# Kernel optimization log

Measured on AMD Instinct MI355X. Metric: run time of the kernel, lower is better.

The kernel has to match this reference:

```python
import jax, jax.numpy as jnp
import numpy as np

B, H, S, D = 4, 16, 2048, 64

def setup_inputs() -> dict:
    key = jax.random.key(0)
    kq, kk, kv = jax.random.split(key, 3)
    q = jax.random.normal(kq, (B, H, S, D), dtype=jnp.float32)
    k = jax.random.normal(kk, (B, H, S, D), dtype=jnp.float32)
    v = jax.random.normal(kv, (B, H, S, D), dtype=jnp.float32)
    return {"q": q, "k": k, "v": v}

def reference(q, k, v):
    # Faithful port of TransformerBlock.scaled_dot_product_attention
    # (is_causal=True, mha_dropout=0.0 / eval mode).
    head_dim = q.shape[-1]
    scale = jnp.asarray(head_dim, q.dtype) ** -0.5
    q_len, k_len = q.shape[-2], k.shape[-2]
    # causal additive bias: 0 on/below diagonal, -inf above
    causal = jnp.tril(jnp.ones((q_len, k_len), dtype=bool))
    attn_bias = jnp.where(causal, jnp.asarray(0.0, q.dtype), jnp.asarray(-jnp.inf, q.dtype))
    # [b,h,s,d] x [b,h,t,d] -> [b,h,s,t]
    attn_weights = jnp.einsum('bhsd,bhtd->bhst', q * scale, k) + attn_bias
    attn = jax.nn.softmax(attn_weights, axis=-1)
    out = jnp.einsum('bhst,bhtd->bhsd', attn, v)
    return out
```

## Files before the change

kernel.cpp:

```cpp
#include <hip/hip_runtime.h>
#include <math.h>


#define S_LEN 2048
#define D_DIM 64
#define TK 64
#define LSTR 72
#define MNEG -30000.0f

typedef __attribute__((ext_vector_type(8))) short bf16x8;
typedef __attribute__((ext_vector_type(4))) float f32x4;

static __device__ __forceinline__ float fast_exp2(float x) {
#if __has_builtin(__builtin_amdgcn_exp2f)
    return __builtin_amdgcn_exp2f(x);
#else
    float r;
    asm volatile("v_exp_f32 %0, %1\n\ts_nop 1" : "=v"(r) : "v"(x));
    return r;
#endif
}

static __device__ __forceinline__ unsigned int pack_bf16(float a, float b) {
    union { float f; unsigned int u; } ca, cb;
    ca.f = a; cb.f = b;
    unsigned int ua = ca.u + 0x8000u;
    unsigned int ub = cb.u + 0x8000u;
    return (ua >> 16) | (ub & 0xFFFF0000u);
}

__global__ __launch_bounds__(256, 4)
void fa_fwd(const float* __restrict__ qg,
            const float* __restrict__ kg,
            const float* __restrict__ vg,
            float* __restrict__ og)
{
    const int head = blockIdx.x;
    const int pr   = blockIdx.y;
    const int tid  = threadIdx.x;
    const int wave = tid >> 6;
    const int lane = tid & 63;
    const int m16  = lane & 15;
    const int quad = lane >> 4;

    __shared__ unsigned short Kl[TK][LSTR];
    __shared__ unsigned short Vt[D_DIM][LSTR];
    __shared__ unsigned short Pl[4][16][LSTR];

    const size_t hoff = (size_t)head * S_LEN * D_DIM;
    const float* kh = kg + hoff;
    const float* vh = vg + hoff;

    const int ksr = tid >> 2;
    const int ksc = (tid & 3) << 4;
    const int va  = lane >> 3;
    const int vb  = lane & 7;
    const int vrr = wave * 16 + 2 * vb;
    const int vcc = 8 * va;
    const float LOG2E = 1.4426950408889634f;

    for (int pass = 0; pass < 2; ++pass) {
        const int q0 = ((pass == 0) ? pr : (31 - pr)) * TK;

        bf16x8 qf[2];
        {
            const float* qp = qg + hoff + (size_t)(q0 + wave * 16 + m16) * D_DIM + quad * 8;
            #pragma unroll
            for (int c = 0; c < 2; ++c) {
                float4 a = reinterpret_cast<const float4*>(qp + c * 32)[0];
                float4 b = reinterpret_cast<const float4*>(qp + c * 32)[1];
                unsigned int u0 = pack_bf16(a.x * 0.125f, a.y * 0.125f);
                unsigned int u1 = pack_bf16(a.z * 0.125f, a.w * 0.125f);
                unsigned int u2 = pack_bf16(b.x * 0.125f, b.y * 0.125f);
                unsigned int u3 = pack_bf16(b.z * 0.125f, b.w * 0.125f);
                qf[c][0] = (short)(u0 & 0xFFFF); qf[c][1] = (short)(u0 >> 16);
                qf[c][2] = (short)(u1 & 0xFFFF); qf[c][3] = (short)(u1 >> 16);
                qf[c][4] = (short)(u2 & 0xFFFF); qf[c][5] = (short)(u2 >> 16);
                qf[c][6] = (short)(u3 & 0xFFFF); qf[c][7] = (short)(u3 >> 16);
            }
        }

        float m_i = MNEG, l_i = 0.f;
        f32x4 oacc[4];
        #pragma unroll
        for (int nc = 0; nc < 4; ++nc) oacc[nc] = (f32x4){0.f, 0.f, 0.f, 0.f};

        float4 kA, kB, kC, kD, vA, vB, vC, vD;
        {
            const float* kp = kh + (size_t)ksr * D_DIM + ksc;
            kA = reinterpret_cast<const float4*>(kp)[0];
            kB = reinterpret_cast<const float4*>(kp)[1];
            kC = reinterpret_cast<const float4*>(kp)[2];
            kD = reinterpret_cast<const float4*>(kp)[3];
            const float* vp = vh + (size_t)vrr * D_DIM + vcc;
            vA = reinterpret_cast<const float4*>(vp)[0];
            vB = reinterpret_cast<const float4*>(vp)[1];
            vC = reinterpret_cast<const float4*>(vp + D_DIM)[0];
            vD = reinterpret_cast<const float4*>(vp + D_DIM)[1];
        }

        for (int j0 = 0; j0 <= q0; j0 += TK) {
            __syncthreads();
            {
                uint4 w0, w1;
                w0.x = pack_bf16(kA.x, kA.y); w0.y = pack_bf16(kA.z, kA.w);
                w0.z = pack_bf16(kB.x, kB.y); w0.w = pack_bf16(kB.z, kB.w);
                w1.x = pack_bf16(kC.x, kC.y); w1.y = pack_bf16(kC.z, kC.w);
                w1.z = pack_bf16(kD.x, kD.y); w1.w = pack_bf16(kD.z, kD.w);
                *reinterpret_cast<uint4*>(&Kl[ksr][ksc])     = w0;
                *reinterpret_cast<uint4*>(&Kl[ksr][ksc + 8]) = w1;

                float r0[8] = {vA.x, vA.y, vA.z, vA.w, vB.x, vB.y, vB.z, vB.w};
                float r1[8] = {vC.x, vC.y, vC.z, vC.w, vD.x, vD.y, vD.z, vD.w};
                #pragma unroll
                for (int jj = 0; jj < 8; ++jj) {
                    int j = (jj + va) & 7;
                    *reinterpret_cast<unsigned int*>(&Vt[vcc + j][vrr]) = pack_bf16(r0[j], r1[j]);
                }
            }
            __syncthreads();

            if (j0 + TK <= q0) {
                const float* kp = kh + (size_t)(j0 + TK + ksr) * D_DIM + ksc;
                kA = reinterpret_cast<const float4*>(kp)[0];
                kB = reinterpret_cast<const float4*>(kp)[1];
                kC = reinterpret_cast<const float4*>(kp)[2];
                kD = reinterpret_cast<const float4*>(kp)[3];
                const float* vp = vh + (size_t)(j0 + TK + vrr) * D_DIM + vcc;
                vA = reinterpret_cast<const float4*>(vp)[0];
                vB = reinterpret_cast<const float4*>(vp)[1];
                vC = reinterpret_cast<const float4*>(vp + D_DIM)[0];
                vD = reinterpret_cast<const float4*>(vp + D_DIM)[1];
            }

            float sv[4][4];
            #pragma unroll
            for (int nt = 0; nt < 4; ++nt) {
                f32x4 acc = (f32x4){0.f, 0.f, 0.f, 0.f};
                bf16x8 kf0 = *reinterpret_cast<const bf16x8*>(&Kl[nt * 16 + m16][quad * 8]);
                bf16x8 kf1 = *reinterpret_cast<const bf16x8*>(&Kl[nt * 16 + m16][32 + quad * 8]);
                acc = __builtin_amdgcn_mfma_f32_16x16x32_bf16(kf0, qf[0], acc, 0, 0, 0);
                acc = __builtin_amdgcn_mfma_f32_16x16x32_bf16(kf1, qf[1], acc, 0, 0, 0);
                #pragma unroll
                for (int r = 0; r < 4; ++r) sv[nt][r] = acc[r];
            }

            if (j0 == q0) {
                #pragma unroll
                for (int nt = 0; nt < 4; ++nt)
                    #pragma unroll
                    for (int r = 0; r < 4; ++r)
                        if (nt * 16 + quad * 4 + r > wave * 16 + m16) sv[nt][r] = MNEG;
            }

            float a0 = fmaxf(fmaxf(sv[0][0], sv[0][1]), fmaxf(sv[0][2], sv[0][3]));
            float a1 = fmaxf(fmaxf(sv[1][0], sv[1][1]), fmaxf(sv[1][2], sv[1][3]));
            float a2 = fmaxf(fmaxf(sv[2][0], sv[2][1]), fmaxf(sv[2][2], sv[2][3]));
            float a3 = fmaxf(fmaxf(sv[3][0], sv[3][1]), fmaxf(sv[3][2], sv[3][3]));
            float rm = fmaxf(fmaxf(a0, a1), fmaxf(a2, a3));
            rm = fmaxf(rm, __shfl_xor(rm, 16, 64));
            rm = fmaxf(rm, __shfl_xor(rm, 32, 64));
            float mnew  = fmaxf(m_i, rm);
            float alpha = fast_exp2((m_i - mnew) * LOG2E);
            float msc   = mnew * LOG2E;
            m_i = mnew;

            float rs = 0.f;
            #pragma unroll
            for (int nt = 0; nt < 4; ++nt) {
                float e0 = fast_exp2(fmaf(sv[nt][0], LOG2E, -msc));
                float e1 = fast_exp2(fmaf(sv[nt][1], LOG2E, -msc));
                float e2 = fast_exp2(fmaf(sv[nt][2], LOG2E, -msc));
                float e3 = fast_exp2(fmaf(sv[nt][3], LOG2E, -msc));
                rs += (e0 + e1) + (e2 + e3);
                uint2 pw;
                pw.x = pack_bf16(e0, e1);
                pw.y = pack_bf16(e2, e3);
                *reinterpret_cast<uint2*>(&Pl[wave][m16][nt * 16 + quad * 4]) = pw;
            }
            rs += __shfl_xor(rs, 16, 64);
            rs += __shfl_xor(rs, 32, 64);
            l_i = fmaf(alpha, l_i, rs);

            #pragma unroll
            for (int nc = 0; nc < 4; ++nc)
                #pragma unroll
                for (int r = 0; r < 4; ++r)
                    oacc[nc][r] *= alpha;

            asm volatile("s_waitcnt lgkmcnt(0)" ::: "memory");

            bf16x8 pf0 = *reinterpret_cast<const bf16x8*>(&Pl[wave][m16][quad * 8]);
            bf16x8 pf1 = *reinterpret_cast<const bf16x8*>(&Pl[wave][m16][32 + quad * 8]);
            #pragma unroll
            for (int nc = 0; nc < 4; ++nc) {
                bf16x8 vf0 = *reinterpret_cast<const bf16x8*>(&Vt[nc * 16 + m16][quad * 8]);
                bf16x8 vf1 = *reinterpret_cast<const bf16x8*>(&Vt[nc * 16 + m16][32 + quad * 8]);
                oacc[nc] = __builtin_amdgcn_mfma_f32_16x16x32_bf16(vf0, pf0, oacc[nc], 0, 0, 0);
                oacc[nc] = __builtin_amdgcn_mfma_f32_16x16x32_bf16(vf1, pf1, oacc[nc], 0, 0, 0);
            }
        }

        float inv = 1.0f / l_i;
        float* op = og + hoff + (size_t)(q0 + wave * 16 + m16) * D_DIM;
        #pragma unroll
        for (int nc = 0; nc < 4; ++nc) {
            float4 o4;
            o4.x = oacc[nc][0] * inv;
            o4.y = oacc[nc][1] * inv;
            o4.z = oacc[nc][2] * inv;
            o4.w = oacc[nc][3] * inv;
            reinterpret_cast<float4*>(op + nc * 16 + quad * 4)[0] = o4;
        }
    }
}

extern "C" void kernel_launch(void* const* d_in, const int* in_sizes, int n_in,
                              void* d_out, int out_size, void* d_ws, size_t ws_size,
                              hipStream_t stream) {
    const float* q = (const float*)d_in[0];
    const float* k = (const float*)d_in[1];
    const float* v = (const float*)d_in[2];
    float* o = (float*)d_out;
    dim3 grid(64 , 16 );
    fa_fwd<<<grid, 256, 0, stream>>>(q, k, v, o);
}
```

Measured before the change: 225.6 us.

## Pre-convert K/V to swizzled bf16 in workspace and double-buffer via direct LDS loads

Adds a prep kernel that converts K to bf16 with an XOR-swizzled layout and transposes V into bf16 tiles, writing both to the workspace. The attention kernel then streams these tiles straight into LDS with global_load_lds, double-buffered so the next tile's load overlaps compute. This removes the per-block fp32-to-bf16 conversion and register staging of K/V that every query block repeated, and halves K/V read bytes. The cost is an extra launch plus a full K/V read and write pass. The old kernel is kept as a fallback when workspace is too small.

After: 207.2 us. 8.2% less time.

```diff
diff --git a/kernel.cpp b/kernel.cpp
--- a/kernel.cpp
+++ b/kernel.cpp
@@ -5,8 +5,10 @@
 #define S_LEN 2048
 #define D_DIM 64
 #define TK 64
+#define NHEAD 64
+#define MNEG -30000.0f
 #define LSTR 72
-#define MNEG -30000.0f
+#define PREP_KBLK 4096
 
 typedef __attribute__((ext_vector_type(8))) short bf16x8;
 typedef __attribute__((ext_vector_type(4))) float f32x4;
@@ -29,11 +31,238 @@
     return (ua >> 16) | (ub & 0xFFFF0000u);
 }
 
+typedef const __attribute__((address_space(1))) unsigned int* gas1_t;
+typedef __attribute__((address_space(3))) unsigned int* las3_t;
+static __device__ __forceinline__ void stage16(const void* g, void* l) {
+    __builtin_amdgcn_global_load_lds((gas1_t)g, (las3_t)l, 16, 0, 0);
+}
+
+__global__ __launch_bounds__(256)
+void fa_prep(const float* __restrict__ kg, const float* __restrict__ vg,
+             unsigned short* __restrict__ kb, unsigned short* __restrict__ vb)
+{
+    const int tid = threadIdx.x;
+    const int bid = blockIdx.x;
+    if (bid < PREP_KBLK) {
+        const int cid = bid * 256 + tid;
+        const int ch  = cid & 7;
+        const int row = cid >> 3;
+        const int kv  = row & (S_LEN - 1);
+        const float4* s = reinterpret_cast<const float4*>(kg + (size_t)row * D_DIM + ch * 8);
+        float4 a = s[0], b = s[1];
+        uint4 w;
+        w.x = pack_bf16(a.x, a.y); w.y = pack_bf16(a.z, a.w);
+        w.z = pack_bf16(b.x, b.y); w.w = pack_bf16(b.z, b.w);
+        const int dst = ch ^ (kv & 7);
+        *reinterpret_cast<uint4*>(kb + (size_t)row * D_DIM + dst * 8) = w;
+    } else {
+        const int wv   = (bid - PREP_KBLK) * 4 + (tid >> 6);
+        const int lane = tid & 63;
+        const int kg8  = lane >> 3;
+        const int dg   = lane & 7;
+        const float* s = vg + ((size_t)wv * TK + kg8 * 8) * D_DIM + dg * 8;
+        float va[8][8];
+        #pragma unroll
+        for (int i = 0; i < 8; ++i) {
+            const float4* sp = reinterpret_cast<const float4*>(s + (size_t)i * D_DIM);
+            float4 x = sp[0], y = sp[1];
+            va[i][0] = x.x; va[i][1] = x.y; va[i][2] = x.z; va[i][3] = x.w;
+            va[i][4] = y.x; va[i][5] = y.y; va[i][6] = y.z; va[i][7] = y.w;
+        }
+        unsigned short* db = vb + (size_t)wv * (TK * D_DIM);
+        #pragma unroll
+        for (int j = 0; j < 8; ++j) {
+            const int d = dg * 8 + j;
+            uint4 w;
+            w.x = pack_bf16(va[0][j], va[1][j]);
+            w.y = pack_bf16(va[2][j], va[3][j]);
+            w.z = pack_bf16(va[4][j], va[5][j]);
+            w.w = pack_bf16(va[6][j], va[7][j]);
+            *reinterpret_cast<uint4*>(db + d * D_DIM + 8 * (kg8 ^ j)) = w;
+        }
+    }
+}
+
 __global__ __launch_bounds__(256, 4)
 void fa_fwd(const float* __restrict__ qg,
-            const float* __restrict__ kg,
-            const float* __restrict__ vg,
+            const unsigned short* __restrict__ kb,
+            const unsigned short* __restrict__ vb,
             float* __restrict__ og)
+{
+    const int head = blockIdx.x;
+    const int pr   = blockIdx.y;
+    const int tid  = threadIdx.x;
+    const int wave = tid >> 6;
+    const int lane = tid & 63;
+    const int m16  = lane & 15;
+    const int quad = lane >> 4;
+
+    __shared__ unsigned short Kl[2][TK * D_DIM];
+    __shared__ unsigned short Vt[2][TK * D_DIM];
+    __shared__ unsigned short Pl[4][16 * TK];
+
+    const size_t hoff = (size_t)head * S_LEN * D_DIM;
+    const unsigned short* kbh = kb + hoff;
+    const unsigned short* vbh = vb + hoff;
+    float* __restrict__ ogh = og + hoff;
+
+    const int swz  = (m16 & 7) << 4;
+    const int colA = (quad * 16) ^ swz;
+    const int colB = (64 + quad * 16) ^ swz;
+    const int rowB = m16 * 128;
+    const int sgo  = wave * 512 + lane * 8;
+
+    char* klds = (char*)&Kl[0][0];
+    char* vlds = (char*)&Vt[0][0];
+    char* plds = (char*)&Pl[0][0] + wave * 2048 + m16 * 128;
+    char* kw   = klds + wave * 1024;
+    char* vw   = vlds + wave * 1024;
+
+    const float QSC = 0.18033688011112042f;
+
+    for (int pass = 0; pass < 2; ++pass) {
+        const int q0 = ((pass == 0) ? pr : (31 - pr)) * TK;
+        const int T  = q0 >> 6;
+
+        bf16x8 qf[2];
+        {
+            const float* qp = qg + hoff + (size_t)(q0 + wave * 16 + m16) * D_DIM + quad * 8;
+            #pragma unroll
+            for (int c = 0; c < 2; ++c) {
+                float4 a = reinterpret_cast<const float4*>(qp + c * 32)[0];
+                float4 b = reinterpret_cast<const float4*>(qp + c * 32)[1];
+                unsigned int u0 = pack_bf16(a.x * QSC, a.y * QSC);
+                unsigned int u1 = pack_bf16(a.z * QSC, a.w * QSC);
+                unsigned int u2 = pack_bf16(b.x * QSC, b.y * QSC);
+                unsigned int u3 = pack_bf16(b.z * QSC, b.w * QSC);
+                qf[c][0] = (short)(u0 & 0xFFFF); qf[c][1] = (short)(u0 >> 16);
+                qf[c][2] = (short)(u1 & 0xFFFF); qf[c][3] = (short)(u1 >> 16);
+                qf[c][4] = (short)(u2 & 0xFFFF); qf[c][5] = (short)(u2 >> 16);
+                qf[c][6] = (short)(u3 & 0xFFFF); qf[c][7] = (short)(u3 >> 16);
+            }
+        }
+
+        float m_i = MNEG, l_i = 0.f;
+        f32x4 oacc[4];
+        #pragma unroll
+        for (int nc = 0; nc < 4; ++nc) oacc[nc] = (f32x4){0.f, 0.f, 0.f, 0.f};
+
+        {
+            const unsigned short* ks = kbh + sgo;
+            const unsigned short* vs = vbh + sgo;
+            stage16(ks,        kw);
+            stage16(ks + 2048, kw + 4096);
+            stage16(vs,        vw);
+            stage16(vs + 2048, vw + 4096);
+        }
+        __syncthreads();
+
+        int cur = 0;
+        for (int t = 0; t <= T; ++t) {
+            if (t < T) {
+                const unsigned short* ks = kbh + (size_t)(t + 1) * 4096 + sgo;
+                const unsigned short* vs = vbh + (size_t)(t + 1) * 4096 + sgo;
+                const int nb = (cur ^ 1) * 8192;
+                stage16(ks,        kw + nb);
+                stage16(ks + 2048, kw + nb + 4096);
+                stage16(vs,        vw + nb);
+                stage16(vs + 2048, vw + nb + 4096);
+            }
+
+            const char* kt = klds + cur * 8192;
+            const char* vt = vlds + cur * 8192;
+
+            float sv[4][4];
+            #pragma unroll
+            for (int nt = 0; nt < 4; ++nt) {
+                f32x4 acc = (f32x4){0.f, 0.f, 0.f, 0.f};
+                const char* kr = kt + nt * 2048 + rowB;
+                bf16x8 kf0 = *reinterpret_cast<const bf16x8*>(kr + colA);
+                bf16x8 kf1 = *reinterpret_cast<const bf16x8*>(kr + colB);
+                acc = __builtin_amdgcn_mfma_f32_16x16x32_bf16(kf0, qf[0], acc, 0, 0, 0);
+                acc = __builtin_amdgcn_mfma_f32_16x16x32_bf16(kf1, qf[1], acc, 0, 0, 0);
+                #pragma unroll
+                for (int r = 0; r < 4; ++r) sv[nt][r] = acc[r];
+            }
+
+            if (t == T) {
+                #pragma unroll
+                for (int nt = 0; nt < 4; ++nt)
+                    #pragma unroll
+                    for (int r = 0; r < 4; ++r)
+                        if (nt * 16 + quad * 4 + r > wave * 16 + m16) sv[nt][r] = MNEG;
+            }
+
+            float a0 = fmaxf(fmaxf(sv[0][0], sv[0][1]), fmaxf(sv[0][2], sv[0][3]));
+            float a1 = fmaxf(fmaxf(sv[1][0], sv[1][1]), fmaxf(sv[1][2], sv[1][3]));
+            float a2 = fmaxf(fmaxf(sv[2][0], sv[2][1]), fmaxf(sv[2][2], sv[2][3]));
+            float a3 = fmaxf(fmaxf(sv[3][0], sv[3][1]), fmaxf(sv[3][2], sv[3][3]));
+            float rm = fmaxf(fmaxf(a0, a1), fmaxf(a2, a3));
+            rm = fmaxf(rm, __shfl_xor(rm, 16, 64));
+            rm = fmaxf(rm, __shfl_xor(rm, 32, 64));
+            float mnew  = fmaxf(m_i, rm);
+            float alpha = fast_exp2(m_i - mnew);
+            m_i = mnew;
+
+            float rs = 0.f;
+            #pragma unroll
+            for (int nt = 0; nt < 4; ++nt) {
+                float e0 = fast_exp2(sv[nt][0] - m_i);
+                float e1 = fast_exp2(sv[nt][1] - m_i);
+                float e2 = fast_exp2(sv[nt][2] - m_i);
+                float e3 = fast_exp2(sv[nt][3] - m_i);
+                rs += (e0 + e1) + (e2 + e3);
+                uint2 pw;
+                pw.x = pack_bf16(e0, e1);
+                pw.y = pack_bf16(e2, e3);
+                *reinterpret_cast<uint2*>(plds + ((nt * 32 + quad * 8) ^ swz)) = pw;
+            }
+            rs += __shfl_xor(rs, 16, 64);
+            rs += __shfl_xor(rs, 32, 64);
+            l_i = fmaf(alpha, l_i, rs);
+
+            #pragma unroll
+            for (int nc = 0; nc < 4; ++nc)
+                #pragma unroll
+                for (int r = 0; r < 4; ++r)
+                    oacc[nc][r] *= alpha;
+
+            asm volatile("s_waitcnt lgkmcnt(0)" ::: "memory");
+
+            bf16x8 pf0 = *reinterpret_cast<const bf16x8*>(plds + colA);
+            bf16x8 pf1 = *reinterpret_cast<const bf16x8*>(plds + colB);
+            #pragma unroll
+            for (int nc = 0; nc < 4; ++nc) {
+                const char* vr = vt + nc * 2048 + rowB;
+                bf16x8 vf0 = *reinterpret_cast<const bf16x8*>(vr + colA);
+                bf16x8 vf1 = *reinterpret_cast<const bf16x8*>(vr + colB);
+                oacc[nc] = __builtin_amdgcn_mfma_f32_16x16x32_bf16(vf0, pf0, oacc[nc], 0, 0, 0);
+                oacc[nc] = __builtin_amdgcn_mfma_f32_16x16x32_bf16(vf1, pf1, oacc[nc], 0, 0, 0);
+            }
+
+            __syncthreads();
+            cur ^= 1;
+        }
+
+        float inv = 1.0f / l_i;
+        float* op = ogh + (size_t)(q0 + wave * 16 + m16) * D_DIM;
+        #pragma unroll
+        for (int nc = 0; nc < 4; ++nc) {
+            float4 o4;
+            o4.x = oacc[nc][0] * inv;
+            o4.y = oacc[nc][1] * inv;
+            o4.z = oacc[nc][2] * inv;
+            o4.w = oacc[nc][3] * inv;
+            reinterpret_cast<float4*>(op + nc * 16 + quad * 4)[0] = o4;
+        }
+    }
+}
+
+__global__ __launch_bounds__(256, 4)
+void fa_fwd_fb(const float* __restrict__ qg,
+               const float* __restrict__ kg,
+               const float* __restrict__ vg,
+               float* __restrict__ og)
 {
     const int head = blockIdx.x;
     const int pr   = blockIdx.y;
@@ -222,6 +451,15 @@
     const float* k = (const float*)d_in[1];
     const float* v = (const float*)d_in[2];
     float* o = (float*)d_out;
-    dim3 grid(64 , 16 );
-    fa_fwd<<<grid, 256, 0, stream>>>(q, k, v, o);
-}
+    const size_t kvShorts = (size_t)NHEAD * S_LEN * D_DIM;
+    const size_t wsNeed   = 2 * kvShorts * sizeof(unsigned short);
+    dim3 grid(NHEAD, 16);
+    if (d_ws != nullptr && ws_size >= wsNeed) {
+        unsigned short* kb = (unsigned short*)d_ws;
+        unsigned short* vb = kb + kvShorts;
+        fa_prep<<<PREP_KBLK + 512, 256, 0, stream>>>(k, v, kb, vb);
+        fa_fwd<<<grid, 256, 0, stream>>>(q, kb, vb, o);
+    } else {
+        fa_fwd_fb<<<grid, 256, 0, stream>>>(q, k, v, o);
+    }
+}
```
